# Optimization experiments

Hardware: AMD Instinct MI355X
Metric: run time of the kernel (lower is better)

The kernel has to match this reference:

```python
import jax, jax.numpy as jnp
import numpy as np

D_MODEL, D_EDGE, D_STRUCT = 128, 64, 8
N, E, B = 50000, 800000, 1

def _lin(key, din, dout):
    kw, kb = jax.random.split(key)
    s = 1.0 / np.sqrt(din)
    return (jax.random.uniform(kw, (din, dout), jnp.float32, -s, s),
            jax.random.uniform(kb, (dout,), jnp.float32, -s, s))

def setup_inputs() -> dict:
    key = jax.random.key(0)
    ks = jax.random.split(key, 16)
    H = jax.random.normal(ks[0], (B, N, D_MODEL), jnp.float32)
    xyz = jax.random.normal(ks[1], (B, N, 3), jnp.float32)
    edge_index = jax.random.randint(ks[2], (2, E), 0, N, jnp.int64)
    edge_struct = jax.random.normal(ks[3], (E, D_STRUCT), jnp.float32)
    edge_rest_lengths = jax.random.uniform(ks[4], (E,), jnp.float32)
    We1, be1 = _lin(ks[5], 2 * D_MODEL + 2 + D_STRUCT, D_EDGE)
    We2, be2 = _lin(ks[6], D_EDGE, D_EDGE)
    Wg1, bg1 = _lin(ks[7], 2 + D_STRUCT, 32)
    Wg2, bg2 = _lin(ks[8], 32, 1)
    Wn1, bn1 = _lin(ks[9], D_MODEL + D_EDGE, 2 * D_MODEL)
    Wn2, bn2 = _lin(ks[10], 2 * D_MODEL, D_MODEL)
    ln_g = jnp.ones((D_MODEL,), jnp.float32)
    ln_b = jnp.zeros((D_MODEL,), jnp.float32)
    return dict(H=H, xyz=xyz, edge_index=edge_index, edge_struct=edge_struct,
                edge_rest_lengths=edge_rest_lengths,
                We1=We1, be1=be1, We2=We2, be2=be2,
                Wg1=Wg1, bg1=bg1, Wg2=Wg2, bg2=bg2,
                Wn1=Wn1, bn1=bn1, Wn2=Wn2, bn2=bn2,
                ln_g=ln_g, ln_b=ln_b)

def reference(H, xyz, edge_index, edge_struct, edge_rest_lengths,
              We1, be1, We2, be2, Wg1, bg1, Wg2, bg2,
              Wn1, bn1, Wn2, bn2, ln_g, ln_b):
    Bn, Nn, d = H.shape
    i, j = edge_index[0], edge_index[1]
    # edge geometry
    diff = xyz[:, i, :] - xyz[:, j, :]                      # (B,E,3)
    dist2 = jnp.sum(diff * diff, axis=-1, keepdims=True)    # (B,E,1)
    dist = jnp.sqrt(dist2 + 1e-9)
    rest = edge_rest_lengths.reshape(1, -1, 1)
    delta = (dist - rest) / (rest + 1e-9)
    struct = jnp.broadcast_to(edge_struct[None], (Bn, edge_struct.shape[0], edge_struct.shape[1]))
    # edge message MLP
    Hi, Hj = H[:, i, :], H[:, j, :]
    e_in = jnp.concatenate([Hi, Hj, dist2, delta, struct], axis=-1)  # (B,E,2d+2+ds)
    e = jax.nn.silu(e_in @ We1 + be1)
    e_msg = jax.nn.silu(e @ We2 + be2)                       # (B,E,d_edge)
    # gate
    g_in = jnp.concatenate([dist2, delta, struct], axis=-1)
    g = jax.nn.sigmoid(jax.nn.silu(g_in @ Wg1 + bg1) @ Wg2 + bg2)  # (B,E,1)
    e_msg = e_msg * g
    # scatter-add aggregate to destination node i
    agg = jnp.zeros((Bn, Nn, e_msg.shape[-1]), H.dtype).at[:, i, :].add(e_msg)
    # node MLP (dropout is identity at eval) + residual + LayerNorm
    n_in = jnp.concatenate([H, agg], axis=-1)
    upd = jax.nn.silu(n_in @ Wn1 + bn1) @ Wn2 + bn2
    x = H + upd
    mu = jnp.mean(x, axis=-1, keepdims=True)
    var = jnp.mean((x - mu) ** 2, axis=-1, keepdims=True)
    return (x - mu) / jnp.sqrt(var + 1e-5) * ln_g + ln_b
```

## Files before the change

kernel.cpp:

```cpp
#include <hip/hip_runtime.h>
#include <stdint.h>

#define N_NODES 50000
#define N_EDGES 800000
#define NODE_TILES 782

#define SE   72
#define SW2  72
#define SPQ  136
#define SN1  216
#define SN2  280
#define ATS  40
#define MSTR 72

#define EC_GRID 962
#define EC_CHUNK 13

#define SCAN_B 98

typedef short bf16x8 __attribute__((ext_vector_type(8)));
typedef short short4v __attribute__((ext_vector_type(4)));
typedef unsigned short ushort8 __attribute__((ext_vector_type(8)));
typedef float f32x4  __attribute__((ext_vector_type(4)));

static __device__ __forceinline__ unsigned short f2bf(float f) {
  unsigned int x = __float_as_uint(f);
  unsigned int r = (x + 0x7fffu + ((x >> 16) & 1u)) >> 16;
  return (unsigned short)r;
}
static __device__ __forceinline__ float bf2f(unsigned short u) {
  return __uint_as_float(((unsigned int)u) << 16);
}
static __device__ __forceinline__ float silu_f(float x) {
  return x * __builtin_amdgcn_rcpf(1.0f + __expf(-x));
}
static __device__ __forceinline__ float sigmoid_f(float x) {
  return __builtin_amdgcn_rcpf(1.0f + __expf(-x));
}
static __device__ __forceinline__ unsigned int cvt_pk_bf16(float lo, float hi) {
  unsigned int r;
  asm("v_cvt_pk_bf16_f32 %0, %1, %2" : "=v"(r) : "v"(lo), "v"(hi));
  return r;
}
static __device__ __forceinline__ bf16x8 pack8(float4 u, float4 v) {
  bf16x8 w;
  w[0] = (short)f2bf(u.x); w[1] = (short)f2bf(u.y);
  w[2] = (short)f2bf(u.z); w[3] = (short)f2bf(u.w);
  w[4] = (short)f2bf(v.x); w[5] = (short)f2bf(v.y);
  w[6] = (short)f2bf(v.z); w[7] = (short)f2bf(v.w);
  return w;
}

__global__ void prep_hist(
    const int* __restrict__ eidx,
    const float* __restrict__ We1, const float* __restrict__ be1,
    const float* __restrict__ We2,
    const float* __restrict__ Wn1, const float* __restrict__ Wn2,
    unsigned short* __restrict__ WpqT, unsigned short* __restrict__ We2T,
    unsigned short* __restrict__ Wn1T, unsigned short* __restrict__ Wn2T,
    unsigned short* __restrict__ WrT,
    int* __restrict__ cnt)
{
  const int gid = blockIdx.x * 256 + threadIdx.x;
  const int gsz = gridDim.x * 256;
  for (int i = gid; i < 128 * SPQ; i += gsz) {
    int n = i / SPQ, k = i % SPQ;
    unsigned short v = 0;
    if (k < 128) v = (n < 64) ? f2bf(We1[k * 64 + n]) : f2bf(We1[(128 + k) * 64 + (n - 64)]);
    WpqT[i] = v;
  }
  for (int i = gid; i < 64 * SW2; i += gsz) {
    int n = i / SW2, k = i % SW2;
    We2T[i] = (k < 64) ? f2bf(We2[k * 64 + n]) : (unsigned short)0;
  }
  for (int i = gid; i < 256 * SN1; i += gsz) {
    int n = i / SN1, k = i % SN1;
    Wn1T[i] = (k < 192) ? f2bf(Wn1[k * 256 + n]) : (unsigned short)0;
  }
  for (int i = gid; i < 128 * SN2; i += gsz) {
    int n = i / SN2, k = i % SN2;
    Wn2T[i] = (k < 256) ? f2bf(Wn2[k * 128 + n]) : (unsigned short)0;
  }
  for (int i = gid; i < 64 * 32; i += gsz) {
    int n = i >> 5, k = i & 31;
    float v = 0.f;
    if (k < 2)       v = We1[256 * 64 + n];
    else if (k < 4)  v = We1[257 * 64 + n];
    else if (k < 12) v = We1[(258 + (k - 4)) * 64 + n];
    else if (k == 12) v = be1[n];
    else if (k == 13) { float w = We1[256 * 64 + n]; v = w - bf2f(f2bf(w)); }
    else if (k == 14) { float w = We1[257 * 64 + n]; v = w - bf2f(f2bf(w)); }
    else if (k == 15) { float w = be1[n];            v = w - bf2f(f2bf(w)); }
    WrT[i] = (k < 16) ? f2bf(v) : (unsigned short)0;
  }
  if (gid < N_EDGES) atomicAdd(&cnt[eidx[gid]], 1);
}

__global__ __launch_bounds__(512) void scan_local(
    const int* __restrict__ cnt, int* __restrict__ rowptr,
    int* __restrict__ bsum)
{
  __shared__ int wsum[8], woff[8];
  const int t = threadIdx.x;
  const int idx = blockIdx.x * 512 + t;
  const int lane = t & 63, wid = t >> 6;
  int c = (idx < N_NODES) ? cnt[idx] : 0;
  int v = c;
  #pragma unroll
  for (int o = 1; o < 64; o <<= 1) {
    int u = __shfl_up(v, o);
    if (lane >= o) v += u;
  }
  if (lane == 63) wsum[wid] = v;
  __syncthreads();
  if (t == 0) {
    int a = 0;
    #pragma unroll
    for (int w = 0; w < 8; ++w) { woff[w] = a; a += wsum[w]; }
    bsum[blockIdx.x] = a;
  }
  __syncthreads();
  if (idx < N_NODES) rowptr[idx] = woff[wid] + (v - c);
}

__global__ __launch_bounds__(128) void scan_mid(
    const int* __restrict__ bsum, int* __restrict__ boff)
{
  __shared__ int ws[2];
  const int t = threadIdx.x;
  const int lane = t & 63, wid = t >> 6;
  int c = (t < SCAN_B) ? bsum[t] : 0;
  int v = c;
  #pragma unroll
  for (int o = 1; o < 64; o <<= 1) {
    int u = __shfl_up(v, o);
    if (lane >= o) v += u;
  }
  if (lane == 63) ws[wid] = v;
  __syncthreads();
  int add = (wid == 1) ? ws[0] : 0;
  if (t < SCAN_B) boff[t] = add + (v - c);
}

__global__ __launch_bounds__(512) void scan_add(
    const int* __restrict__ rowptr, const int* __restrict__ boff,
    int* __restrict__ cursor, float4* __restrict__ agg)
{
  const int idx = blockIdx.x * 512 + threadIdx.x;
  if (idx < N_NODES) cursor[idx] = rowptr[idx] + boff[blockIdx.x];
  if (idx < 50048) {
    float4 z = make_float4(0.f, 0.f, 0.f, 0.f);
    float4* p = agg + (long)idx * 16;
    #pragma unroll
    for (int k = 0; k < 16; ++k) p[k] = z;
  }
}

__global__ void fill_reorder(
    const int* __restrict__ eidx, const float* __restrict__ xyz,
    const float* __restrict__ estruct, const float* __restrict__ erest,
    int* __restrict__ cursor,
    const float* __restrict__ Wg1, const float* __restrict__ bg1,
    const float* __restrict__ Wg2, const float* __restrict__ bg2,
    unsigned short* __restrict__ rec)
{
  int e = blockIdx.x * 256 + threadIdx.x;
  if (e >= N_EDGES) return;
  int i = eidx[e], j = eidx[N_EDGES + e];
  float dx = xyz[i * 3 + 0] - xyz[j * 3 + 0];
  float dy = xyz[i * 3 + 1] - xyz[j * 3 + 1];
  float dz = xyz[i * 3 + 2] - xyz[j * 3 + 2];
  float d2 = dx * dx + dy * dy + dz * dz;
  float dist = sqrtf(d2 + 1e-9f);
  float rest = erest[e];
  float dl = (dist - rest) / (rest + 1e-9f);
  float4 s0 = *(const float4*)&estruct[e * 8];
  float4 s1 = *(const float4*)&estruct[e * 8 + 4];
  float st[8] = {s0.x, s0.y, s0.z, s0.w, s1.x, s1.y, s1.z, s1.w};
  float gsum = 0.f;
  #pragma unroll
  for (int h = 0; h < 32; ++h) {
    float a = bg1[h] + d2 * Wg1[0 * 32 + h] + dl * Wg1[1 * 32 + h];
    #pragma unroll
    for (int c = 0; c < 8; ++c) a += st[c] * Wg1[(2 + c) * 32 + h];
    gsum += silu_f(a) * Wg2[h];
  }
  float g = sigmoid_f(gsum + bg2[0]);

  unsigned short d2h = f2bf(d2);
  unsigned short d2l = f2bf(d2 - bf2f(d2h));
  unsigned short dlh = f2bf(dl);
  unsigned short dll = f2bf(dl - bf2f(dlh));

  ushort8 w0;
  w0[0] = d2h; w0[1] = d2l; w0[2] = dlh; w0[3] = dll;
  w0[4] = f2bf(st[0]); w0[5] = f2bf(st[1]); w0[6] = f2bf(st[2]); w0[7] = f2bf(st[3]);
  uint4 w1;
  w1.x = (unsigned int)f2bf(st[4]) | ((unsigned int)f2bf(st[5]) << 16);
  w1.y = (unsigned int)f2bf(st[6]) | ((unsigned int)f2bf(st[7]) << 16);
  w1.z = __float_as_uint(g);
  w1.w = (unsigned int)i | ((unsigned int)j << 16);

  int pos = atomicAdd(&cursor[i], 1);
  unsigned short* dst = rec + (long)pos * 16;
  *(ushort8*)dst = w0;
  *(uint4*)(dst + 8) = w1;
}

__global__ __launch_bounds__(256, 2) void pq_kernel(
    const float* __restrict__ H, const unsigned short* __restrict__ WpqT,
    unsigned short* __restrict__ P, unsigned short* __restrict__ Q,
    unsigned short* __restrict__ Hbf)
{
  __shared__ unsigned short As[64 * SPQ];
  __shared__ unsigned short Ws[128 * SPQ];

  const int tid  = threadIdx.x;
  const int lane = tid & 63;
  const int wv   = tid >> 6;
  const int lr   = lane & 15;
  const int lq   = lane >> 4;
  const int m0   = wv * 16;

  for (int i = tid * 8; i < 128 * SPQ; i += 256 * 8)
    *(bf16x8*)&Ws[i] = *(const bf16x8*)&WpqT[i];

  f32x4 zero4 = {0.f, 0.f, 0.f, 0.f};
  for (int t = blockIdx.x; t < NODE_TILES; t += 512) {
    const int n0 = t * 64;
    __syncthreads();
    {
      int le = tid >> 2, q = tid & 3;
      int node = n0 + le; if (node >= N_NODES) node = N_NODES - 1;
      const float* src = H + (long)node * 128 + q * 32;
      unsigned short* dst = &As[le * SPQ + q * 32];
      #pragma unroll
      for (int c = 0; c < 32; c += 8) {
        float4 u = *(const float4*)(src + c);
        float4 v = *(const float4*)(src + c + 4);
        *(bf16x8*)(dst + c) = pack8(u, v);
      }
    }
    __syncthreads();

    for (int idx = tid * 8; idx < 64 * 128; idx += 256 * 8) {
      int row = idx >> 7, col = idx & 127;
      *(bf16x8*)&Hbf[((long)n0 + row) * 128 + col] = *(const bf16x8*)&As[row * SPQ + col];
    }

    f32x4 acc[8];
    #pragma unroll
    for (int f = 0; f < 8; ++f) acc[f] = zero4;
    #pragma unroll
    for (int s = 0; s < 4; ++s) {
      int kb = s * 32 + lq * 8;
      bf16x8 a = *(const bf16x8*)&As[(m0 + lr) * SPQ + kb];
      #pragma unroll
      for (int f = 0; f < 8; ++f) {
        bf16x8 b = *(const bf16x8*)&Ws[(f * 16 + lr) * SPQ + kb];
        acc[f] = __builtin_amdgcn_mfma_f32_16x16x32_bf16(a, b, acc[f], 0, 0, 0);
      }
    }
    #pragma unroll
    for (int f = 0; f < 8; ++f) {
      #pragma unroll
      for (int r = 0; r < 4; ++r) {
        int node = n0 + m0 + lq * 4 + r;
        if (node < N_NODES) {
          if (f < 4) P[(long)node * 64 + f * 16 + lr] = f2bf(acc[f][r]);
          else       Q[(long)node * 64 + (f - 4) * 16 + lr] = f2bf(acc[f][r]);
        }
      }
    }
  }
}

__global__ __launch_bounds__(256, 4) void edge_compute(
    const unsigned short* __restrict__ P, const unsigned short* __restrict__ Q,
    const unsigned short* __restrict__ rec,
    const unsigned short* __restrict__ We2T, const float* __restrict__ be2,
    const unsigned short* __restrict__ WrT,
    float* __restrict__ agg)
{
  __shared__ unsigned short W2s[64 * SW2];
  __shared__ unsigned short Es [4 * 16 * SE];
  __shared__ unsigned short At [4 * 16 * ATS];
  __shared__ unsigned short Ms [4 * 16 * MSTR];

  const int tid  = threadIdx.x;
  const int lane = tid & 63;
  const int wv   = tid >> 6;
  const int lr   = lane & 15;
  const int lq   = lane >> 4;

  for (int i = tid * 8; i < 64 * SW2; i += 256 * 8)
    *(bf16x8*)&W2s[i] = *(const bf16x8*)&We2T[i];

  unsigned short* Es_w = &Es[wv * 16 * SE];
  unsigned short* At_w = &At[wv * 16 * ATS];
  unsigned short* Ms_w = &Ms[wv * 16 * MSTR];

  if (lane < 16) {
    ushort8 z;
    #pragma unroll
    for (int c = 0; c < 8; ++c) z[c] = 0;
    *(ushort8*)&At_w[lane * ATS + 16] = z;
    *(ushort8*)&At_w[lane * ATS + 24] = z;
  }

  bf16x8 aWr[4];
  float bias2[4][4];
  #pragma unroll
  for (int f = 0; f < 4; ++f) {
    aWr[f] = *(const bf16x8*)&WrT[(f * 16 + lr) * 32 + lq * 8];
    #pragma unroll
    for (int r = 0; r < 4; ++r) bias2[f][r] = be2[f * 16 + lq * 4 + r];
  }
  __syncthreads();

  const int n_tiles = N_EDGES / 16;
  const int wid = blockIdx.x * 4 + wv;
  const int t0 = wid * EC_CHUNK;
  const int t1 = (t0 + EC_CHUNK < n_tiles) ? (t0 + EC_CHUNK) : n_tiles;
  if (t0 >= n_tiles) return;

  f32x4 zero4 = {0.f, 0.f, 0.f, 0.f};
  int   cur_node;
  {
    int ij0 = *(const int*)(rec + (long)t0 * 16 * 16 + 14);
    cur_node = ij0 & 0xffff;
  }
  float acc        = 0.f;
  bool  use_atomic = true;

  for (int tile = t0; tile < t1; ++tile) {
    const int s0 = tile * 16;

    const unsigned short* rp = rec + (long)(s0 + lr) * 16;
    ushort8 ra = *(const ushort8*)rp;
    uint4   rb = *(const uint4*)(rp + 8);
    float g     = __uint_as_float(rb.z);
    int   inode = rb.w & 0xffff;
    int   jnode = (rb.w >> 16) & 0xffff;

    if (lane < 16) {
      ushort8 w1;
      w1[0] = (unsigned short)(rb.x & 0xffff);
      w1[1] = (unsigned short)(rb.x >> 16);
      w1[2] = (unsigned short)(rb.y & 0xffff);
      w1[3] = (unsigned short)(rb.y >> 16);
      w1[4] = 0x3F80u; w1[5] = (unsigned short)ra[0];
      w1[6] = (unsigned short)ra[2]; w1[7] = 0x3F80u;
      *(ushort8*)&At_w[lane * ATS]     = ra;
      *(ushort8*)&At_w[lane * ATS + 8] = w1;
    }

    bf16x8 bA = *(const bf16x8*)&At_w[lr * ATS + lq * 8];
    f32x4 acc1[4];
    #pragma unroll
    for (int f = 0; f < 4; ++f)
      acc1[f] = __builtin_amdgcn_mfma_f32_16x16x32_bf16(aWr[f], bA, zero4, 0, 0, 0);

    const unsigned short* Pb = P + (long)inode * 64;
    const unsigned short* Qb = Q + (long)jnode * 64;
    #pragma unroll
    for (int f = 0; f < 4; ++f) {
      short4v pv = *(const short4v*)&Pb[f * 16 + lq * 4];
      short4v qv = *(const short4v*)&Qb[f * 16 + lq * 4];
      float v0 = silu_f(bf2f((unsigned short)pv[0]) + bf2f((unsigned short)qv[0]) + acc1[f][0]);
      float v1 = silu_f(bf2f((unsigned short)pv[1]) + bf2f((unsigned short)qv[1]) + acc1[f][1]);
      float v2 = silu_f(bf2f((unsigned short)pv[2]) + bf2f((unsigned short)qv[2]) + acc1[f][2]);
      float v3 = silu_f(bf2f((unsigned short)pv[3]) + bf2f((unsigned short)qv[3]) + acc1[f][3]);
      uint2 w;
      w.x = cvt_pk_bf16(v0, v1);
      w.y = cvt_pk_bf16(v2, v3);
      *(uint2*)&Es_w[lr * SE + f * 16 + lq * 4] = w;
    }

    f32x4 acc2[4];
    #pragma unroll
    for (int f = 0; f < 4; ++f) acc2[f] = zero4;
    #pragma unroll
    for (int s = 0; s < 2; ++s) {
      int kb = s * 32 + lq * 8;
      bf16x8 bE = *(const bf16x8*)&Es_w[lr * SE + kb];
      #pragma unroll
      for (int f = 0; f < 4; ++f) {
        bf16x8 aW = *(const bf16x8*)&W2s[(f * 16 + lr) * SW2 + kb];
        acc2[f] = __builtin_amdgcn_mfma_f32_16x16x32_bf16(aW, bE, acc2[f], 0, 0, 0);
      }
    }

    #pragma unroll
    for (int f = 0; f < 4; ++f) {
      float o0 = silu_f(acc2[f][0] + bias2[f][0]) * g;
      float o1 = silu_f(acc2[f][1] + bias2[f][1]) * g;
      float o2 = silu_f(acc2[f][2] + bias2[f][2]) * g;
      float o3 = silu_f(acc2[f][3] + bias2[f][3]) * g;
      uint2 w;
      w.x = cvt_pk_bf16(o0, o1);
      w.y = cvt_pk_bf16(o2, o3);
      *(uint2*)&Ms_w[lr * MSTR + f * 16 + lq * 4] = w;
    }

    #pragma unroll
    for (int e = 0; e < 16; ++e) {
      int ie = __builtin_amdgcn_readlane(inode, e);
      if (ie != cur_node) {
        if (use_atomic) atomicAdd(&agg[(long)cur_node * 64 + lane], acc);
        else            agg[(long)cur_node * 64 + lane] = acc;
        use_atomic = false;
        cur_node = ie;
        acc = 0.f;
      }
      acc += bf2f(Ms_w[e * MSTR + lane]);
    }
  }
  atomicAdd(&agg[(long)cur_node * 64 + lane], acc);
}

__global__ __launch_bounds__(256, 2) void h1_kernel(
    const unsigned short* __restrict__ Hbf, const float* __restrict__ agg,
    const unsigned short* __restrict__ Wn1T, const float* __restrict__ bn1,
    unsigned short* __restrict__ h1)
{
  __shared__ unsigned short Wl[128 * SN1];

  const int tid  = threadIdx.x;
  const int lane = tid & 63;
  const int wv   = tid >> 6;
  const int lr   = lane & 15;
  const int lq   = lane >> 4;
  const int m0   = wv * 16;
  const int p    = blockIdx.x & 1;

  for (int i = tid * 8; i < 128 * SN1; i += 256 * 8)
    *(bf16x8*)&Wl[i] = *(const bf16x8*)&Wn1T[p * 128 * SN1 + i];
  __syncthreads();

  f32x4 zero4 = {0.f, 0.f, 0.f, 0.f};
  for (int t = blockIdx.x >> 1; t < NODE_TILES; t += 256) {
    const int n0 = t * 64;
    int rowa = n0 + m0 + lr;
    int rowc = rowa < N_NODES ? rowa : N_NODES - 1;

    f32x4 acc1[8];
    #pragma unroll
    for (int f = 0; f < 8; ++f) acc1[f] = zero4;
    #pragma unroll
    for (int s = 0; s < 6; ++s) {
      int kb = s * 32 + lq * 8;
      bf16x8 a;
      if (s < 4) {
        a = *(const bf16x8*)&Hbf[(long)rowa * 128 + kb];
      } else {
        const float* pp = agg + (long)rowc * 64 + (kb - 128);
        float4 u = *(const float4*)pp;
        float4 v = *(const float4*)(pp + 4);
        a = pack8(u, v);
      }
      #pragma unroll
      for (int f = 0; f < 8; ++f) {
        bf16x8 b = *(const bf16x8*)&Wl[(f * 16 + lr) * SN1 + kb];
        acc1[f] = __builtin_amdgcn_mfma_f32_16x16x32_bf16(a, b, acc1[f], 0, 0, 0);
      }
    }
    #pragma unroll
    for (int f = 0; f < 8; ++f) {
      int col = p * 128 + f * 16 + lr;
      float bias = bn1[col];
      #pragma unroll
      for (int r = 0; r < 4; ++r) {
        int node = n0 + m0 + lq * 4 + r;
        h1[(long)node * 256 + col] = f2bf(silu_f(acc1[f][r] + bias));
      }
    }
  }
}

__global__ __launch_bounds__(256, 2) void out_kernel(
    const float* __restrict__ H, const unsigned short* __restrict__ h1,
    const unsigned short* __restrict__ Wn2T, const float* __restrict__ bn2,
    const float* __restrict__ ln_g, const float* __restrict__ ln_b,
    float* __restrict__ out)
{
  __shared__ unsigned short Wl[128 * SN2];

  const int tid  = threadIdx.x;
  const int lane = tid & 63;
  const int wv   = tid >> 6;
  const int lr   = lane & 15;
  const int lq   = lane >> 4;
  const int m0   = wv * 16;

  for (int i = tid * 8; i < 128 * SN2; i += 256 * 8)
    *(bf16x8*)&Wl[i] = *(const bf16x8*)&Wn2T[i];
  __syncthreads();

  f32x4 zero4 = {0.f, 0.f, 0.f, 0.f};
  for (int t = blockIdx.x; t < NODE_TILES; t += 512) {
    const int n0 = t * 64;
    int rowa = n0 + m0 + lr;

    f32x4 acc2[8];
    #pragma unroll
    for (int f = 0; f < 8; ++f) acc2[f] = zero4;
    #pragma unroll
    for (int s = 0; s < 8; ++s) {
      int kb = s * 32 + lq * 8;
      bf16x8 a = *(const bf16x8*)&h1[(long)rowa * 256 + kb];
      #pragma unroll
      for (int f = 0; f < 8; ++f) {
        bf16x8 b = *(const bf16x8*)&Wl[(f * 16 + lr) * SN2 + kb];
        acc2[f] = __builtin_amdgcn_mfma_f32_16x16x32_bf16(a, b, acc2[f], 0, 0, 0);
      }
    }

    #pragma unroll
    for (int r = 0; r < 4; ++r) {
      int node = n0 + m0 + lq * 4 + r;
      int nc = node < N_NODES ? node : N_NODES - 1;
      float x[8];
      float sum = 0.f, sumsq = 0.f;
      #pragma unroll
      for (int f = 0; f < 8; ++f) {
        int n = f * 16 + lr;
        float u = acc2[f][r] + bn2[n];
        float xv = H[(long)nc * 128 + n] + u;
        x[f] = xv;
        sum += xv;
        sumsq += xv * xv;
      }
      #pragma unroll
      for (int o = 1; o < 16; o <<= 1) {
        sum   += __shfl_xor(sum, o);
        sumsq += __shfl_xor(sumsq, o);
      }
      float mu  = sum * (1.f / 128.f);
      float var = sumsq * (1.f / 128.f) - mu * mu;
      float rstd = rsqrtf(var + 1e-5f);
      if (node < N_NODES) {
        #pragma unroll
        for (int f = 0; f < 8; ++f) {
          int n = f * 16 + lr;
          out[(long)node * 128 + n] = (x[f] - mu) * rstd * ln_g[n] + ln_b[n];
        }
      }
    }
  }
}

extern "C" void kernel_launch(void* const* d_in, const int* in_sizes, int n_in,
                              void* d_out, int out_size, void* d_ws, size_t ws_size,
                              hipStream_t stream) {
  const float* H       = (const float*)d_in[0];
  const float* xyz     = (const float*)d_in[1];
  const int*   eidx    = (const int*)d_in[2];
  const float* estruct = (const float*)d_in[3];
  const float* erest   = (const float*)d_in[4];
  const float* We1     = (const float*)d_in[5];
  const float* be1     = (const float*)d_in[6];
  const float* We2     = (const float*)d_in[7];
  const float* be2     = (const float*)d_in[8];
  const float* Wg1     = (const float*)d_in[9];
  const float* bg1     = (const float*)d_in[10];
  const float* Wg2     = (const float*)d_in[11];
  const float* bg2     = (const float*)d_in[12];
  const float* Wn1     = (const float*)d_in[13];
  const float* bn1     = (const float*)d_in[14];
  const float* Wn2     = (const float*)d_in[15];
  const float* bn2     = (const float*)d_in[16];
  const float* ln_g    = (const float*)d_in[17];
  const float* ln_b    = (const float*)d_in[18];

  char* ws = (char*)d_ws;
  float*          agg    = (float*)(ws + 0);
  unsigned short* Hbf    = (unsigned short*)(ws + 12812288);
  unsigned short* rec    = (unsigned short*)(ws + 25624576);
  unsigned short* P      = (unsigned short*)(ws + 51224576);
  unsigned short* Qm     = (unsigned short*)(ws + 57624576);
  int*            cnt    = (int*)(ws + 64024576);
  int*            rowptr = (int*)(ws + 64224768);
  int*            cursor = (int*)(ws + 64424960);
  unsigned short* WpqT   = (unsigned short*)(ws + 64625152);
  unsigned short* We2T   = (unsigned short*)(ws + 64659968);
  unsigned short* Wn1T   = (unsigned short*)(ws + 64669184);
  unsigned short* Wn2T   = (unsigned short*)(ws + 64779776);
  unsigned short* WrT    = (unsigned short*)(ws + 64851456);
  int*            bsum   = (int*)(ws + 64855552);
  int*            boff   = (int*)(ws + 64856064);
  unsigned short* h1     = (unsigned short*)(ws + 64856576);
  float* out = (float*)d_out;

  hipMemsetAsync(cnt, 0, (size_t)N_NODES * sizeof(int), stream);

  hipLaunchKernelGGL(prep_hist, dim3(3125), dim3(256), 0, stream,
                     eidx, We1, be1, We2, Wn1, Wn2, WpqT, We2T, Wn1T, Wn2T, WrT, cnt);
  hipLaunchKernelGGL(scan_local, dim3(SCAN_B), dim3(512), 0, stream,
                     cnt, rowptr, bsum);
  hipLaunchKernelGGL(scan_mid, dim3(1), dim3(128), 0, stream,
                     bsum, boff);
  hipLaunchKernelGGL(scan_add, dim3(SCAN_B), dim3(512), 0, stream,
                     rowptr, boff, cursor, (float4*)agg);
  hipLaunchKernelGGL(fill_reorder, dim3(3125), dim3(256), 0, stream,
                     eidx, xyz, estruct, erest, cursor,
                     Wg1, bg1, Wg2, bg2, rec);
  hipLaunchKernelGGL(pq_kernel, dim3(512), dim3(256), 0, stream,
                     H, WpqT, P, Qm, Hbf);
  hipLaunchKernelGGL(edge_compute, dim3(EC_GRID), dim3(256), 0, stream,
                     P, Qm, rec, We2T, be2, WrT, agg);
  hipLaunchKernelGGL(h1_kernel, dim3(512), dim3(256), 0, stream,
                     Hbf, agg, Wn1T, bn1, h1);
  hipLaunchKernelGGL(out_kernel, dim3(512), dim3(256), 0, stream,
                     H, h1, Wn2T, bn2, ln_g, ln_b, out);
}
```

Measured before the change: 368.2 us.

## Write edge records in original order and gather via sorted index permutation

```diff
diff --git a/kernel.cpp b/kernel.cpp
--- a/kernel.cpp
+++ b/kernel.cpp
@@ -156,13 +156,13 @@
   }
 }
 
-__global__ void fill_reorder(
+__global__ void fill_gate(
     const int* __restrict__ eidx, const float* __restrict__ xyz,
     const float* __restrict__ estruct, const float* __restrict__ erest,
     int* __restrict__ cursor,
     const float* __restrict__ Wg1, const float* __restrict__ bg1,
     const float* __restrict__ Wg2, const float* __restrict__ bg2,
-    unsigned short* __restrict__ rec)
+    unsigned short* __restrict__ rec_e, int* __restrict__ order)
 {
   int e = blockIdx.x * 256 + threadIdx.x;
   if (e >= N_EDGES) return;
@@ -201,10 +201,12 @@
   w1.z = __float_as_uint(g);
   w1.w = (unsigned int)i | ((unsigned int)j << 16);
 
-  int pos = atomicAdd(&cursor[i], 1);
-  unsigned short* dst = rec + (long)pos * 16;
+  unsigned short* dst = rec_e + (long)e * 16;
   *(ushort8*)dst = w0;
   *(uint4*)(dst + 8) = w1;
+
+  int pos = atomicAdd(&cursor[i], 1);
+  order[pos] = e;
 }
 
 __global__ __launch_bounds__(256, 2) void pq_kernel(
@@ -277,7 +279,7 @@
 
 __global__ __launch_bounds__(256, 4) void edge_compute(
     const unsigned short* __restrict__ P, const unsigned short* __restrict__ Q,
-    const unsigned short* __restrict__ rec,
+    const int* __restrict__ order, const unsigned short* __restrict__ rec_e,
     const unsigned short* __restrict__ We2T, const float* __restrict__ be2,
     const unsigned short* __restrict__ WrT,
     float* __restrict__ agg)
@@ -325,23 +327,19 @@
   if (t0 >= n_tiles) return;
 
   f32x4 zero4 = {0.f, 0.f, 0.f, 0.f};
-  int   cur_node;
-  {
-    int ij0 = *(const int*)(rec + (long)t0 * 16 * 16 + 14);
-    cur_node = ij0 & 0xffff;
-  }
+
+  int eid = order[t0 * 16 + lr];
+  ushort8 ra = *(const ushort8*)(rec_e + (long)eid * 16);
+  uint4   rb = *(const uint4*)(rec_e + (long)eid * 16 + 8);
+
+  int   cur_node   = __builtin_amdgcn_readlane((int)rb.w, 0) & 0xffff;
   float acc        = 0.f;
   bool  use_atomic = true;
 
   for (int tile = t0; tile < t1; ++tile) {
-    const int s0 = tile * 16;
-
-    const unsigned short* rp = rec + (long)(s0 + lr) * 16;
-    ushort8 ra = *(const ushort8*)rp;
-    uint4   rb = *(const uint4*)(rp + 8);
     float g     = __uint_as_float(rb.z);
-    int   inode = rb.w & 0xffff;
-    int   jnode = (rb.w >> 16) & 0xffff;
+    int   inode = (int)(rb.w & 0xffff);
+    int   jnode = (int)((rb.w >> 16) & 0xffff);
 
     if (lane < 16) {
       ushort8 w1;
@@ -353,6 +351,13 @@
       w1[6] = (unsigned short)ra[2]; w1[7] = 0x3F80u;
       *(ushort8*)&At_w[lane * ATS]     = ra;
       *(ushort8*)&At_w[lane * ATS + 8] = w1;
+    }
+
+    ushort8 ra_n = ra; uint4 rb_n = rb;
+    if (tile + 1 < t1) {
+      int eid_n = order[(tile + 1) * 16 + lr];
+      ra_n = *(const ushort8*)(rec_e + (long)eid_n * 16);
+      rb_n = *(const uint4*)(rec_e + (long)eid_n * 16 + 8);
     }
 
     bf16x8 bA = *(const bf16x8*)&At_w[lr * ATS + lq * 8];
@@ -403,18 +408,29 @@
       *(uint2*)&Ms_w[lr * MSTR + f * 16 + lq * 4] = w;
     }
 
+    float mv[16];
+    #pragma unroll
+    for (int e = 0; e < 16; ++e) mv[e] = bf2f(Ms_w[e * MSTR + lane]);
+
+    int up = __shfl_up(inode, 1);
+    unsigned long long bm = __ballot(inode != up);
+    unsigned mask = (unsigned)bm & 0xFFFEu;
+    int i0 = __builtin_amdgcn_readlane(inode, 0);
+    if (i0 != cur_node) mask |= 1u;
+
     #pragma unroll
     for (int e = 0; e < 16; ++e) {
-      int ie = __builtin_amdgcn_readlane(inode, e);
-      if (ie != cur_node) {
+      if (mask & (1u << e)) {
         if (use_atomic) atomicAdd(&agg[(long)cur_node * 64 + lane], acc);
         else            agg[(long)cur_node * 64 + lane] = acc;
         use_atomic = false;
-        cur_node = ie;
+        cur_node = __builtin_amdgcn_readlane(inode, e);
         acc = 0.f;
       }
-      acc += bf2f(Ms_w[e * MSTR + lane]);
-    }
+      acc += mv[e];
+    }
+
+    ra = ra_n; rb = rb_n;
   }
   atomicAdd(&agg[(long)cur_node * 64 + lane], acc);
 }
@@ -576,20 +592,21 @@
   char* ws = (char*)d_ws;
   float*          agg    = (float*)(ws + 0);
   unsigned short* Hbf    = (unsigned short*)(ws + 12812288);
-  unsigned short* rec    = (unsigned short*)(ws + 25624576);
-  unsigned short* P      = (unsigned short*)(ws + 51224576);
-  unsigned short* Qm     = (unsigned short*)(ws + 57624576);
-  int*            cnt    = (int*)(ws + 64024576);
-  int*            rowptr = (int*)(ws + 64224768);
-  int*            cursor = (int*)(ws + 64424960);
-  unsigned short* WpqT   = (unsigned short*)(ws + 64625152);
-  unsigned short* We2T   = (unsigned short*)(ws + 64659968);
-  unsigned short* Wn1T   = (unsigned short*)(ws + 64669184);
-  unsigned short* Wn2T   = (unsigned short*)(ws + 64779776);
-  unsigned short* WrT    = (unsigned short*)(ws + 64851456);
-  int*            bsum   = (int*)(ws + 64855552);
-  int*            boff   = (int*)(ws + 64856064);
-  unsigned short* h1     = (unsigned short*)(ws + 64856576);
+  unsigned short* rec_e  = (unsigned short*)(ws + 25624576);
+  int*            order  = (int*)(ws + 51224576);
+  unsigned short* P      = (unsigned short*)(ws + 54424576);
+  unsigned short* Qm     = (unsigned short*)(ws + 60824576);
+  int*            cnt    = (int*)(ws + 67224576);
+  int*            rowptr = (int*)(ws + 67424768);
+  int*            cursor = (int*)(ws + 67624960);
+  unsigned short* WpqT   = (unsigned short*)(ws + 67825152);
+  unsigned short* We2T   = (unsigned short*)(ws + 67859968);
+  unsigned short* Wn1T   = (unsigned short*)(ws + 67869184);
+  unsigned short* Wn2T   = (unsigned short*)(ws + 67979776);
+  unsigned short* WrT    = (unsigned short*)(ws + 68051456);
+  int*            bsum   = (int*)(ws + 68055552);
+  int*            boff   = (int*)(ws + 68056064);
+  unsigned short* h1     = (unsigned short*)(ws + 68056576);
   float* out = (float*)d_out;
 
   hipMemsetAsync(cnt, 0, (size_t)N_NODES * sizeof(int), stream);
@@ -602,13 +619,13 @@
                      bsum, boff);
   hipLaunchKernelGGL(scan_add, dim3(SCAN_B), dim3(512), 0, stream,
                      rowptr, boff, cursor, (float4*)agg);
-  hipLaunchKernelGGL(fill_reorder, dim3(3125), dim3(256), 0, stream,
+  hipLaunchKernelGGL(fill_gate, dim3(3125), dim3(256), 0, stream,
                      eidx, xyz, estruct, erest, cursor,
-                     Wg1, bg1, Wg2, bg2, rec);
+                     Wg1, bg1, Wg2, bg2, rec_e, order);
   hipLaunchKernelGGL(pq_kernel, dim3(512), dim3(256), 0, stream,
                      H, WpqT, P, Qm, Hbf);
   hipLaunchKernelGGL(edge_compute, dim3(EC_GRID), dim3(256), 0, stream,
-                     P, Qm, rec, We2T, be2, WrT, agg);
+                     P, Qm, order, rec_e, We2T, be2, WrT, agg);
   hipLaunchKernelGGL(h1_kernel, dim3(512), dim3(256), 0, stream,
                      Hbf, agg, Wn1T, bn1, h1);
   hipLaunchKernelGGL(out_kernel, dim3(512), dim3(256), 0, stream,
```

Measured after the change: 370.9 us. No clear change (+0.7%).

## Merge fill_reorder and pq_kernel into one launch; ballot-based segment detection in edge_compute

Applied to the files above, without the earlier changes.

```diff
diff --git a/kernel.cpp b/kernel.cpp
--- a/kernel.cpp
+++ b/kernel.cpp
@@ -17,6 +17,10 @@
 #define EC_CHUNK 13
 
 #define SCAN_B 98
+
+#define FP_PQ_BLOCKS 256
+#define FP_GRID 2048
+#define FP_FILL_STRIDE ((FP_GRID - FP_PQ_BLOCKS) * 256)
 
 typedef short bf16x8 __attribute__((ext_vector_type(8)));
 typedef short short4v __attribute__((ext_vector_type(4)));
@@ -156,7 +160,10 @@
   }
 }
 
-__global__ void fill_reorder(
+__global__ __launch_bounds__(256, 3) void fill_pq(
+    const float* __restrict__ H, const unsigned short* __restrict__ WpqT,
+    unsigned short* __restrict__ P, unsigned short* __restrict__ Q,
+    unsigned short* __restrict__ Hbf,
     const int* __restrict__ eidx, const float* __restrict__ xyz,
     const float* __restrict__ estruct, const float* __restrict__ erest,
     int* __restrict__ cursor,
@@ -164,113 +171,111 @@
     const float* __restrict__ Wg2, const float* __restrict__ bg2,
     unsigned short* __restrict__ rec)
 {
-  int e = blockIdx.x * 256 + threadIdx.x;
-  if (e >= N_EDGES) return;
-  int i = eidx[e], j = eidx[N_EDGES + e];
-  float dx = xyz[i * 3 + 0] - xyz[j * 3 + 0];
-  float dy = xyz[i * 3 + 1] - xyz[j * 3 + 1];
-  float dz = xyz[i * 3 + 2] - xyz[j * 3 + 2];
-  float d2 = dx * dx + dy * dy + dz * dz;
-  float dist = sqrtf(d2 + 1e-9f);
-  float rest = erest[e];
-  float dl = (dist - rest) / (rest + 1e-9f);
-  float4 s0 = *(const float4*)&estruct[e * 8];
-  float4 s1 = *(const float4*)&estruct[e * 8 + 4];
-  float st[8] = {s0.x, s0.y, s0.z, s0.w, s1.x, s1.y, s1.z, s1.w};
-  float gsum = 0.f;
-  #pragma unroll
-  for (int h = 0; h < 32; ++h) {
-    float a = bg1[h] + d2 * Wg1[0 * 32 + h] + dl * Wg1[1 * 32 + h];
-    #pragma unroll
-    for (int c = 0; c < 8; ++c) a += st[c] * Wg1[(2 + c) * 32 + h];
-    gsum += silu_f(a) * Wg2[h];
-  }
-  float g = sigmoid_f(gsum + bg2[0]);
-
-  unsigned short d2h = f2bf(d2);
-  unsigned short d2l = f2bf(d2 - bf2f(d2h));
-  unsigned short dlh = f2bf(dl);
-  unsigned short dll = f2bf(dl - bf2f(dlh));
-
-  ushort8 w0;
-  w0[0] = d2h; w0[1] = d2l; w0[2] = dlh; w0[3] = dll;
-  w0[4] = f2bf(st[0]); w0[5] = f2bf(st[1]); w0[6] = f2bf(st[2]); w0[7] = f2bf(st[3]);
-  uint4 w1;
-  w1.x = (unsigned int)f2bf(st[4]) | ((unsigned int)f2bf(st[5]) << 16);
-  w1.y = (unsigned int)f2bf(st[6]) | ((unsigned int)f2bf(st[7]) << 16);
-  w1.z = __float_as_uint(g);
-  w1.w = (unsigned int)i | ((unsigned int)j << 16);
-
-  int pos = atomicAdd(&cursor[i], 1);
-  unsigned short* dst = rec + (long)pos * 16;
-  *(ushort8*)dst = w0;
-  *(uint4*)(dst + 8) = w1;
-}
-
-__global__ __launch_bounds__(256, 2) void pq_kernel(
-    const float* __restrict__ H, const unsigned short* __restrict__ WpqT,
-    unsigned short* __restrict__ P, unsigned short* __restrict__ Q,
-    unsigned short* __restrict__ Hbf)
-{
   __shared__ unsigned short As[64 * SPQ];
   __shared__ unsigned short Ws[128 * SPQ];
 
-  const int tid  = threadIdx.x;
-  const int lane = tid & 63;
-  const int wv   = tid >> 6;
-  const int lr   = lane & 15;
-  const int lq   = lane >> 4;
-  const int m0   = wv * 16;
-
-  for (int i = tid * 8; i < 128 * SPQ; i += 256 * 8)
-    *(bf16x8*)&Ws[i] = *(const bf16x8*)&WpqT[i];
-
-  f32x4 zero4 = {0.f, 0.f, 0.f, 0.f};
-  for (int t = blockIdx.x; t < NODE_TILES; t += 512) {
-    const int n0 = t * 64;
-    __syncthreads();
-    {
-      int le = tid >> 2, q = tid & 3;
-      int node = n0 + le; if (node >= N_NODES) node = N_NODES - 1;
-      const float* src = H + (long)node * 128 + q * 32;
-      unsigned short* dst = &As[le * SPQ + q * 32];
-      #pragma unroll
-      for (int c = 0; c < 32; c += 8) {
-        float4 u = *(const float4*)(src + c);
-        float4 v = *(const float4*)(src + c + 4);
-        *(bf16x8*)(dst + c) = pack8(u, v);
-      }
-    }
-    __syncthreads();
-
-    for (int idx = tid * 8; idx < 64 * 128; idx += 256 * 8) {
-      int row = idx >> 7, col = idx & 127;
-      *(bf16x8*)&Hbf[((long)n0 + row) * 128 + col] = *(const bf16x8*)&As[row * SPQ + col];
-    }
-
-    f32x4 acc[8];
-    #pragma unroll
-    for (int f = 0; f < 8; ++f) acc[f] = zero4;
-    #pragma unroll
-    for (int s = 0; s < 4; ++s) {
-      int kb = s * 32 + lq * 8;
-      bf16x8 a = *(const bf16x8*)&As[(m0 + lr) * SPQ + kb];
+  const int bid = blockIdx.x;
+  const int tid = threadIdx.x;
+
+  if (bid < FP_PQ_BLOCKS) {
+    const int lane = tid & 63;
+    const int wv   = tid >> 6;
+    const int lr   = lane & 15;
+    const int lq   = lane >> 4;
+    const int m0   = wv * 16;
+
+    for (int i = tid * 8; i < 128 * SPQ; i += 256 * 8)
+      *(bf16x8*)&Ws[i] = *(const bf16x8*)&WpqT[i];
+
+    f32x4 zero4 = {0.f, 0.f, 0.f, 0.f};
+    for (int t = bid; t < NODE_TILES; t += FP_PQ_BLOCKS) {
+      const int n0 = t * 64;
+      __syncthreads();
+      {
+        int le = tid >> 2, q = tid & 3;
+        int node = n0 + le; if (node >= N_NODES) node = N_NODES - 1;
+        const float* src = H + (long)node * 128 + q * 32;
+        unsigned short* dst = &As[le * SPQ + q * 32];
+        #pragma unroll
+        for (int c = 0; c < 32; c += 8) {
+          float4 u = *(const float4*)(src + c);
+          float4 v = *(const float4*)(src + c + 4);
+          *(bf16x8*)(dst + c) = pack8(u, v);
+        }
+      }
+      __syncthreads();
+
+      for (int idx = tid * 8; idx < 64 * 128; idx += 256 * 8) {
+        int row = idx >> 7, col = idx & 127;
+        *(bf16x8*)&Hbf[((long)n0 + row) * 128 + col] = *(const bf16x8*)&As[row * SPQ + col];
+      }
+
+      f32x4 acc[8];
+      #pragma unroll
+      for (int f = 0; f < 8; ++f) acc[f] = zero4;
+      #pragma unroll
+      for (int s = 0; s < 4; ++s) {
+        int kb = s * 32 + lq * 8;
+        bf16x8 a = *(const bf16x8*)&As[(m0 + lr) * SPQ + kb];
+        #pragma unroll
+        for (int f = 0; f < 8; ++f) {
+          bf16x8 b = *(const bf16x8*)&Ws[(f * 16 + lr) * SPQ + kb];
+          acc[f] = __builtin_amdgcn_mfma_f32_16x16x32_bf16(a, b, acc[f], 0, 0, 0);
+        }
+      }
       #pragma unroll
       for (int f = 0; f < 8; ++f) {
-        bf16x8 b = *(const bf16x8*)&Ws[(f * 16 + lr) * SPQ + kb];
-        acc[f] = __builtin_amdgcn_mfma_f32_16x16x32_bf16(a, b, acc[f], 0, 0, 0);
-      }
-    }
-    #pragma unroll
-    for (int f = 0; f < 8; ++f) {
-      #pragma unroll
-      for (int r = 0; r < 4; ++r) {
-        int node = n0 + m0 + lq * 4 + r;
-        if (node < N_NODES) {
-          if (f < 4) P[(long)node * 64 + f * 16 + lr] = f2bf(acc[f][r]);
-          else       Q[(long)node * 64 + (f - 4) * 16 + lr] = f2bf(acc[f][r]);
+        #pragma unroll
+        for (int r = 0; r < 4; ++r) {
+          int node = n0 + m0 + lq * 4 + r;
+          if (node < N_NODES) {
+            if (f < 4) P[(long)node * 64 + f * 16 + lr] = f2bf(acc[f][r]);
+            else       Q[(long)node * 64 + (f - 4) * 16 + lr] = f2bf(acc[f][r]);
+          }
         }
       }
+    }
+  } else {
+    for (int e = (bid - FP_PQ_BLOCKS) * 256 + tid; e < N_EDGES; e += FP_FILL_STRIDE) {
+      int i = eidx[e], j = eidx[N_EDGES + e];
+      float dx = xyz[i * 3 + 0] - xyz[j * 3 + 0];
+      float dy = xyz[i * 3 + 1] - xyz[j * 3 + 1];
+      float dz = xyz[i * 3 + 2] - xyz[j * 3 + 2];
+      float d2 = dx * dx + dy * dy + dz * dz;
+      float dist = sqrtf(d2 + 1e-9f);
+      float rest = erest[e];
+      float dl = (dist - rest) / (rest + 1e-9f);
+      float4 s0 = *(const float4*)&estruct[e * 8];
+      float4 s1 = *(const float4*)&estruct[e * 8 + 4];
+      float st[8] = {s0.x, s0.y, s0.z, s0.w, s1.x, s1.y, s1.z, s1.w};
+      float gsum = 0.f;
+      #pragma unroll
+      for (int h = 0; h < 32; ++h) {
+        float a = bg1[h] + d2 * Wg1[0 * 32 + h] + dl * Wg1[1 * 32 + h];
+        #pragma unroll
+        for (int c = 0; c < 8; ++c) a += st[c] * Wg1[(2 + c) * 32 + h];
+        gsum += silu_f(a) * Wg2[h];
+      }
+      float g = sigmoid_f(gsum + bg2[0]);
+
+      unsigned short d2h = f2bf(d2);
+      unsigned short d2l = f2bf(d2 - bf2f(d2h));
+      unsigned short dlh = f2bf(dl);
+      unsigned short dll = f2bf(dl - bf2f(dlh));
+
+      ushort8 w0;
+      w0[0] = d2h; w0[1] = d2l; w0[2] = dlh; w0[3] = dll;
+      w0[4] = f2bf(st[0]); w0[5] = f2bf(st[1]); w0[6] = f2bf(st[2]); w0[7] = f2bf(st[3]);
+      uint4 w1;
+      w1.x = (unsigned int)f2bf(st[4]) | ((unsigned int)f2bf(st[5]) << 16);
+      w1.y = (unsigned int)f2bf(st[6]) | ((unsigned int)f2bf(st[7]) << 16);
+      w1.z = __float_as_uint(g);
+      w1.w = (unsigned int)i | ((unsigned int)j << 16);
+
+      int pos = atomicAdd(&cursor[i], 1);
+      unsigned short* dst = rec + (long)pos * 16;
+      *(ushort8*)dst = w0;
+      *(uint4*)(dst + 8) = w1;
     }
   }
 }
@@ -340,8 +345,8 @@
     ushort8 ra = *(const ushort8*)rp;
     uint4   rb = *(const uint4*)(rp + 8);
     float g     = __uint_as_float(rb.z);
-    int   inode = rb.w & 0xffff;
-    int   jnode = (rb.w >> 16) & 0xffff;
+    int   inode = (int)(rb.w & 0xffff);
+    int   jnode = (int)((rb.w >> 16) & 0xffff);
 
     if (lane < 16) {
       ushort8 w1;
@@ -403,17 +408,26 @@
       *(uint2*)&Ms_w[lr * MSTR + f * 16 + lq * 4] = w;
     }
 
+    float mv[16];
+    #pragma unroll
+    for (int e = 0; e < 16; ++e) mv[e] = bf2f(Ms_w[e * MSTR + lane]);
+
+    int up = __shfl_up(inode, 1);
+    unsigned long long bm = __ballot(inode != up);
+    unsigned mask = (unsigned)bm & 0xFFFEu;
+    int i0 = __builtin_amdgcn_readlane(inode, 0);
+    if (i0 != cur_node) mask |= 1u;
+
     #pragma unroll
     for (int e = 0; e < 16; ++e) {
-      int ie = __builtin_amdgcn_readlane(inode, e);
-      if (ie != cur_node) {
+      if (mask & (1u << e)) {
         if (use_atomic) atomicAdd(&agg[(long)cur_node * 64 + lane], acc);
         else            agg[(long)cur_node * 64 + lane] = acc;
         use_atomic = false;
-        cur_node = ie;
+        cur_node = __builtin_amdgcn_readlane(inode, e);
         acc = 0.f;
       }
-      acc += bf2f(Ms_w[e * MSTR + lane]);
+      acc += mv[e];
     }
   }
   atomicAdd(&agg[(long)cur_node * 64 + lane], acc);
@@ -602,11 +616,10 @@
                      bsum, boff);
   hipLaunchKernelGGL(scan_add, dim3(SCAN_B), dim3(512), 0, stream,
                      rowptr, boff, cursor, (float4*)agg);
-  hipLaunchKernelGGL(fill_reorder, dim3(3125), dim3(256), 0, stream,
+  hipLaunchKernelGGL(fill_pq, dim3(FP_GRID), dim3(256), 0, stream,
+                     H, WpqT, P, Qm, Hbf,
                      eidx, xyz, estruct, erest, cursor,
                      Wg1, bg1, Wg2, bg2, rec);
-  hipLaunchKernelGGL(pq_kernel, dim3(512), dim3(256), 0, stream,
-                     H, WpqT, P, Qm, Hbf);
   hipLaunchKernelGGL(edge_compute, dim3(EC_GRID), dim3(256), 0, stream,
                      P, Qm, rec, We2T, be2, WrT, agg);
   hipLaunchKernelGGL(h1_kernel, dim3(512), dim3(256), 0, stream,
```

Result: slower. 381.0 us (+3.5%).
